# Kernel optimization log

Measured on AMD Instinct MI355X. Metric: run time of the kernel, lower is better.

The kernel has to match this reference:

```python
import jax, jax.numpy as jnp
import numpy as np

H = 128   # hidden_size
B = 8
TQ = 512  # num queries
TK = 512  # num keys


def setup_inputs() -> dict:
    key = jax.random.key(0)
    ks = jax.random.split(key, 8)
    s = 1.0 / np.sqrt(H)  # torch Linear default init bound
    return {
        "queries": jax.random.normal(ks[0], (B, TQ, H), dtype=jnp.float32),
        "keys": jax.random.normal(ks[1], (B, TK, H), dtype=jnp.float32),
        "Wa_w": jax.random.uniform(ks[2], (H, H), jnp.float32, -s, s),
        "Wa_b": jax.random.uniform(ks[3], (H,), jnp.float32, -s, s),
        "Ua_w": jax.random.uniform(ks[4], (H, H), jnp.float32, -s, s),
        "Ua_b": jax.random.uniform(ks[5], (H,), jnp.float32, -s, s),
        "Va_w": jax.random.uniform(ks[6], (H,), jnp.float32, -s, s),
        "Va_b": jax.random.uniform(ks[7], (), jnp.float32, -s, s),
    }


def reference(queries, keys, Wa_w, Wa_b, Ua_w, Ua_b, Va_w, Va_b):
    # Linear projections (torch Linear: y = x @ W.T + b)
    q = queries @ Wa_w.T + Wa_b                  # (B, Tq, H)
    k = keys @ Ua_w.T + Ua_b                     # (B, Tk, H)
    # Additive (Bahdanau) scores with broadcast intermediate (B, Tq, Tk, H)
    e = jnp.tanh(q[:, :, None, :] + k[:, None, :, :])
    scores = jnp.einsum('bqkh,h->bqk', e, Va_w) + Va_b  # (B, Tq, Tk)
    weights = jax.nn.softmax(scores, axis=-1)            # softmax over keys
    contexts = jnp.einsum('bqk,bkh->bqh', weights, keys) # (B, Tq, H)
    return contexts, weights
```

## Files before the change

kernel.cpp:

```cpp
#include <hip/hip_runtime.h>
#include <hip/hip_bf16.h>
#include <stdint.h>

#define HD 128
#define NB 8
#define TQN 512
#define TKN 512
#define QT 8
#define KTILE 64
#define KSTR 132
#define QSTR 132
#define KBSTR 136

typedef __attribute__((ext_vector_type(8))) short short8;
typedef __attribute__((ext_vector_type(4))) float f32x4;

static __device__ __forceinline__ float lo16(uint32_t w){
  union { uint32_t i; float f; } v; v.i = w << 16; return v.f;
}
static __device__ __forceinline__ float hi16(uint32_t w){
  union { uint32_t i; float f; } v; v.i = w & 0xffff0000u; return v.f;
}
static __device__ __forceinline__ float bf2f(unsigned short u){
  union { uint32_t i; float f; } v; v.i = ((uint32_t)u) << 16; return v.f;
}
static __device__ __forceinline__ uint32_t f2bf(float f){
  union { float f; uint32_t i; } v; v.f = f;
  uint32_t u = v.i;
  u += 0x7fffu + ((u >> 16) & 1u);
  return u >> 16;
}

static __device__ __forceinline__ float tanh_acc(float x){
  float e = __builtin_amdgcn_exp2f(x * 2.8853900817779268f);
  return fmaf(-2.0f, __builtin_amdgcn_rcpf(e + 1.0f), 1.0f);
}

template<int CTRL>
static __device__ __forceinline__ float dpp_add(float x){
  union { float f; int i; } u; u.f = x;
  int y = __builtin_amdgcn_update_dpp(0, u.i, CTRL, 0xf, 0xf, true);
  union { int i; float f; } w; w.i = y;
  return x + w.f;
}

static __device__ __forceinline__ float ld1(const void* p, size_t idx, bool f32){
  return f32 ? ((const float*)p)[idx] : bf2f(((const unsigned short*)p)[idx]);
}
static __device__ __forceinline__ short8 ld8bf(const void* p, size_t idx, bool f32){
  short8 r;
  if (f32){
    const float* s = (const float*)p + idx;
    #pragma unroll
    for (int i = 0; i < 8; i++) r[i] = (short)f2bf(s[i]);
  } else {
    r = *(const short8*)((const unsigned short*)p + idx);
  }
  return r;
}

static __device__ __forceinline__ void stage_keys(const void* keys, bool fK,
    unsigned short* keys_s, int b, int kt, int tid){
  if (fK){
    const float4* src = (const float4*)((const float*)keys + (size_t)(b*TKN + kt*KTILE)*HD);
    #pragma unroll
    for (int j = 0; j < 4; j++){
      const int f = tid + 512*j;
      float4 v = src[f];
      const int k = f >> 5;
      const int h = (f & 31) * 4;
      uint2 p;
      p.x = f2bf(v.x) | (f2bf(v.y) << 16);
      p.y = f2bf(v.z) | (f2bf(v.w) << 16);
      *(uint2*)(keys_s + k*KBSTR + h) = p;
    }
  } else {
    const uint4* src = (const uint4*)((const unsigned short*)keys + (size_t)(b*TKN + kt*KTILE)*HD);
    #pragma unroll
    for (int j = 0; j < 2; j++){
      const int f = tid + 512*j;
      uint4 v = src[f];
      const int k = f >> 4;
      const int h = (f & 15) * 8;
      *(uint4*)(keys_s + k*KBSTR + h) = v;
    }
  }
}

__global__ __launch_bounds__(512, 4) void fused_kernel(
    const void* __restrict__ queries, const void* __restrict__ keys,
    const void* __restrict__ Wa_w,   const void* __restrict__ Wa_b,
    const void* __restrict__ Ua_w,   const void* __restrict__ Ua_b,
    const void* __restrict__ Va_w,
    void* __restrict__ out)
{
  __shared__ float qp_s[QT*QSTR];
  __shared__ float va_s[HD];
  __shared__ __align__(16) unsigned short keys_s[KTILE*KBSTR];
  __shared__ __align__(16) float kp_s[KTILE*KSTR];
  __shared__ float sc_s[QT*TKN];
  __shared__ unsigned int flg_s[8];

  const int tid = threadIdx.x;

  if (tid < 8) flg_s[tid] = 0;
  __syncthreads();
  {
    const void* ptrs[7] = {queries, keys, Wa_w, Wa_b, Ua_w, Ua_b, Va_w};
    const int grp = tid >> 5;
    const int l   = tid & 31;
    if (grp < 7){
      const unsigned short* p = (const unsigned short*)ptrs[grp];
      unsigned short a = p[2*l];
      unsigned short c = p[64 + 2*l];
      if (((a >> 7) & 0xFF) > 0x90 || ((c >> 7) & 0xFF) > 0x90)
        atomicOr(&flg_s[grp], 1u);
    }
  }
  __syncthreads();
  const bool fQ  = flg_s[0] != 0;
  const bool fK  = flg_s[1] != 0;
  const bool fWw = flg_s[2] != 0;
  const bool fWb = flg_s[3] != 0;
  const bool fUw = flg_s[4] != 0;
  const bool fUb = flg_s[5] != 0;
  const bool fVw = flg_s[6] != 0;

  const int lane = tid & 63;
  const int wv   = tid >> 6;
  const int ln   = lane & 15;
  const int quad = lane >> 4;
  const int b     = blockIdx.x >> 6;
  const int qbase = (blockIdx.x & 63) * QT;

  if (tid < HD) va_s[tid] = ld1(Va_w, tid, fVw);

  {
    const int h0 = wv * 16;
    const size_t qrow = (size_t)(b*TQN + qbase + (ln & 7))*HD;
    f32x4 c = {0.f,0.f,0.f,0.f};
    #pragma unroll
    for (int ks = 0; ks < 4; ks++){
      short8 a = ld8bf(queries, qrow + ks*32 + quad*8, fQ);
      short8 w = ld8bf(Wa_w, (size_t)(h0 + ln)*HD + ks*32 + quad*8, fWw);
      c = __builtin_amdgcn_mfma_f32_16x16x32_bf16(a, w, c, 0,0,0);
    }
    const float wb = ld1(Wa_b, h0 + ln, fWb);
    #pragma unroll
    for (int r = 0; r < 4; r++){
      const int row = quad*4 + r;
      if (row < QT) qp_s[row*QSTR + h0 + ln] = tanh_acc(c[r] + wb);
    }
  }

  short8 ub[4];
  float ubias;
  {
    const int h0 = wv * 16;
    #pragma unroll
    for (int ks = 0; ks < 4; ks++)
      ub[ks] = ld8bf(Ua_w, (size_t)(h0 + ln)*HD + ks*32 + quad*8, fUw);
    ubias = ld1(Ua_b, h0 + ln, fUb);
  }

  stage_keys(keys, fK, keys_s, b, 0, tid);
  __syncthreads();

  const int s8 = lane >> 3;
  const int o8 = lane & 7;
  float tqr[16], var[16], vat[16];
  {
    const float* qsrc = qp_s + wv*QSTR + o8*16;
    const float* vsrc = va_s + o8*16;
    #pragma unroll
    for (int c = 0; c < 4; c++){
      float4 t = *(const float4*)(qsrc + c*4);
      float4 v = *(const float4*)(vsrc + c*4);
      tqr[c*4+0]=t.x; tqr[c*4+1]=t.y; tqr[c*4+2]=t.z; tqr[c*4+3]=t.w;
      var[c*4+0]=v.x; var[c*4+1]=v.y; var[c*4+2]=v.z; var[c*4+3]=v.w;
      vat[c*4+0]=v.x*t.x; vat[c*4+1]=v.y*t.y; vat[c*4+2]=v.z*t.z; vat[c*4+3]=v.w*t.w;
    }
  }

  for (int kt = 0; kt < 8; kt++){
    f32x4 kc[4];
    #pragma unroll
    for (int mt = 0; mt < 4; mt++) kc[mt] = (f32x4){0.f,0.f,0.f,0.f};
    #pragma unroll
    for (int ks = 0; ks < 4; ks++){
      short8 af[4];
      #pragma unroll
      for (int mt = 0; mt < 4; mt++)
        af[mt] = *(const short8*)(keys_s + (mt*16 + ln)*KBSTR + ks*32 + quad*8);
      #pragma unroll
      for (int mt = 0; mt < 4; mt++)
        kc[mt] = __builtin_amdgcn_mfma_f32_16x16x32_bf16(af[mt], ub[ks], kc[mt], 0,0,0);
    }
    __syncthreads();

    #pragma unroll
    for (int mt = 0; mt < 4; mt++)
      #pragma unroll
      for (int r = 0; r < 4; r++)
        kp_s[(mt*16 + quad*4 + r)*KSTR + wv*16 + ln] = tanh_acc(kc[mt][r] + ubias);
    if (kt < 7) stage_keys(keys, fK, keys_s, b, kt+1, tid);
    __syncthreads();

    float acc[8];
    #pragma unroll
    for (int i = 0; i < 8; i++) acc[i] = 0.f;
    #pragma unroll
    for (int i = 0; i < 8; i++){
      const float* tk = kp_s + (i*8 + s8)*KSTR + o8*16;
      #pragma unroll
      for (int c = 0; c < 4; c++){
        const float4 kv = *(const float4*)(tk + c*4);
        acc[i] = fmaf(fmaf(var[c*4+0], kv.x, vat[c*4+0]),
                      __builtin_amdgcn_rcpf(fmaf(tqr[c*4+0], kv.x, 1.f)), acc[i]);
        acc[i] = fmaf(fmaf(var[c*4+1], kv.y, vat[c*4+1]),
                      __builtin_amdgcn_rcpf(fmaf(tqr[c*4+1], kv.y, 1.f)), acc[i]);
        acc[i] = fmaf(fmaf(var[c*4+2], kv.z, vat[c*4+2]),
                      __builtin_amdgcn_rcpf(fmaf(tqr[c*4+2], kv.z, 1.f)), acc[i]);
        acc[i] = fmaf(fmaf(var[c*4+3], kv.w, vat[c*4+3]),
                      __builtin_amdgcn_rcpf(fmaf(tqr[c*4+3], kv.w, 1.f)), acc[i]);
      }
    }
    #pragma unroll
    for (int i = 0; i < 8; i++){
      float a = acc[i];
      a = dpp_add<0xB1>(a);
      a = dpp_add<0x4E>(a);
      a = dpp_add<0x141>(a);
      acc[i] = a;
    }
    float sc = acc[0];
    #pragma unroll
    for (int i = 1; i < 8; i++) sc = (o8 == i) ? acc[i] : sc;
    sc_s[wv*TKN + kt*KTILE + o8*8 + s8] = sc;
  }
  __syncthreads();

  {
    float vals[8];
    float m = -1e30f;
    #pragma unroll
    for (int j = 0; j < 8; j++){
      vals[j] = sc_s[wv*TKN + lane + 64*j];
      m = fmaxf(m, vals[j]);
    }
    #pragma unroll
    for (int o = 32; o > 0; o >>= 1) m = fmaxf(m, __shfl_xor(m, o));
    float sum = 0.f;
    #pragma unroll
    for (int j = 0; j < 8; j++){
      vals[j] = __builtin_amdgcn_exp2f((vals[j]-m)*1.4426950408889634f);
      sum += vals[j];
    }
    #pragma unroll
    for (int o = 32; o > 0; o >>= 1) sum += __shfl_xor(sum, o);
    const float inv = __builtin_amdgcn_rcpf(sum);
    const size_t wbase = (size_t)NB*TQN*HD + (size_t)(b*TQN + qbase + wv)*TKN;
    #pragma unroll
    for (int j = 0; j < 8; j++){
      const float w = vals[j]*inv;
      sc_s[wv*TKN + lane + 64*j] = w;
      if (fQ) ((float*)out)[wbase + lane + 64*j] = w;
      else    ((unsigned short*)out)[wbase + lane + 64*j] = (unsigned short)f2bf(w);
    }
  }
  __syncthreads();

  {
    const int p2 = wv & 3;
    const int g2 = wv >> 2;
    const int h0 = ln * 8;
    float a0[8], a1[8];
    #pragma unroll
    for (int t = 0; t < 8; t++){ a0[t] = 0.f; a1[t] = 0.f; }
    for (int kt = 0; kt < 8; kt++){
      if (fK){
        const float4* src = (const float4*)((const float*)keys + (size_t)(b*TKN + kt*KTILE)*HD);
        #pragma unroll
        for (int j = 0; j < 4; j++){
          const int f = tid + 512*j;
          const int k = f >> 5;
          const int h = (f & 31) * 4;
          *(float4*)(kp_s + k*KSTR + h) = src[f];
        }
      } else {
        const uint4* src = (const uint4*)((const unsigned short*)keys + (size_t)(b*TKN + kt*KTILE)*HD);
        #pragma unroll
        for (int j = 0; j < 2; j++){
          const int f = tid + 512*j;
          const int k = f >> 4;
          const int h = (f & 15) * 8;
          uint4 v = src[f];
          float4 d0, d1;
          d0.x = lo16(v.x); d0.y = hi16(v.x); d0.z = lo16(v.y); d0.w = hi16(v.y);
          d1.x = lo16(v.z); d1.y = hi16(v.z); d1.z = lo16(v.w); d1.w = hi16(v.w);
          *(float4*)(kp_s + k*KSTR + h)     = d0;
          *(float4*)(kp_s + k*KSTR + h + 4) = d1;
        }
      }
      __syncthreads();
      const float* w0r = sc_s + (2*p2)*TKN + kt*KTILE + g2*32;
      const float* w1r = w0r + TKN;
      #pragma unroll
      for (int i = 0; i < 8; i++){
        const int k = i*4 + quad;
        const float w0 = w0r[k];
        const float w1 = w1r[k];
        const float* kr = kp_s + (g2*32 + k)*KSTR + h0;
        const float4 k0 = *(const float4*)(kr);
        const float4 k1 = *(const float4*)(kr + 4);
        a0[0]=fmaf(w0,k0.x,a0[0]); a0[1]=fmaf(w0,k0.y,a0[1]);
        a0[2]=fmaf(w0,k0.z,a0[2]); a0[3]=fmaf(w0,k0.w,a0[3]);
        a0[4]=fmaf(w0,k1.x,a0[4]); a0[5]=fmaf(w0,k1.y,a0[5]);
        a0[6]=fmaf(w0,k1.z,a0[6]); a0[7]=fmaf(w0,k1.w,a0[7]);
        a1[0]=fmaf(w1,k0.x,a1[0]); a1[1]=fmaf(w1,k0.y,a1[1]);
        a1[2]=fmaf(w1,k0.z,a1[2]); a1[3]=fmaf(w1,k0.w,a1[3]);
        a1[4]=fmaf(w1,k1.x,a1[4]); a1[5]=fmaf(w1,k1.y,a1[5]);
        a1[6]=fmaf(w1,k1.z,a1[6]); a1[7]=fmaf(w1,k1.w,a1[7]);
      }
      __syncthreads();
    }
    #pragma unroll
    for (int t = 0; t < 8; t++){
      a0[t] += __shfl_xor(a0[t], 16); a0[t] += __shfl_xor(a0[t], 32);
      a1[t] += __shfl_xor(a1[t], 16); a1[t] += __shfl_xor(a1[t], 32);
    }
    float* part = qp_s;
    if (g2 == 1 && quad == 0){
      *(float4*)(part + (2*p2  )*HD + h0    ) = (float4){a0[0],a0[1],a0[2],a0[3]};
      *(float4*)(part + (2*p2  )*HD + h0 + 4) = (float4){a0[4],a0[5],a0[6],a0[7]};
      *(float4*)(part + (2*p2+1)*HD + h0    ) = (float4){a1[0],a1[1],a1[2],a1[3]};
      *(float4*)(part + (2*p2+1)*HD + h0 + 4) = (float4){a1[4],a1[5],a1[6],a1[7]};
    }
    __syncthreads();
    if (g2 == 0 && quad == 0){
      const float4 p00 = *(const float4*)(part + (2*p2  )*HD + h0    );
      const float4 p01 = *(const float4*)(part + (2*p2  )*HD + h0 + 4);
      const float4 p10 = *(const float4*)(part + (2*p2+1)*HD + h0    );
      const float4 p11 = *(const float4*)(part + (2*p2+1)*HD + h0 + 4);
      const size_t crow0 = (size_t)(b*TQN + qbase + 2*p2    )*HD + h0;
      const size_t crow1 = (size_t)(b*TQN + qbase + 2*p2 + 1)*HD + h0;
      if (fQ){
        float* oc = (float*)out;
        *(float4*)(oc + crow0)     = (float4){a0[0]+p00.x, a0[1]+p00.y, a0[2]+p00.z, a0[3]+p00.w};
        *(float4*)(oc + crow0 + 4) = (float4){a0[4]+p01.x, a0[5]+p01.y, a0[6]+p01.z, a0[7]+p01.w};
        *(float4*)(oc + crow1)     = (float4){a1[0]+p10.x, a1[1]+p10.y, a1[2]+p10.z, a1[3]+p10.w};
        *(float4*)(oc + crow1 + 4) = (float4){a1[4]+p11.x, a1[5]+p11.y, a1[6]+p11.z, a1[7]+p11.w};
      } else {
        uint4 o0, o1;
        o0.x = f2bf(a0[0]+p00.x) | (f2bf(a0[1]+p00.y) << 16);
        o0.y = f2bf(a0[2]+p00.z) | (f2bf(a0[3]+p00.w) << 16);
        o0.z = f2bf(a0[4]+p01.x) | (f2bf(a0[5]+p01.y) << 16);
        o0.w = f2bf(a0[6]+p01.z) | (f2bf(a0[7]+p01.w) << 16);
        o1.x = f2bf(a1[0]+p10.x) | (f2bf(a1[1]+p10.y) << 16);
        o1.y = f2bf(a1[2]+p10.z) | (f2bf(a1[3]+p10.w) << 16);
        o1.z = f2bf(a1[4]+p11.x) | (f2bf(a1[5]+p11.y) << 16);
        o1.w = f2bf(a1[6]+p11.z) | (f2bf(a1[7]+p11.w) << 16);
        *(uint4*)((unsigned short*)out + crow0) = o0;
        *(uint4*)((unsigned short*)out + crow1) = o1;
      }
    }
  }
}

extern "C" void kernel_launch(void* const* d_in, const int* in_sizes, int n_in,
                              void* d_out, int out_size, void* d_ws, size_t ws_size,
                              hipStream_t stream) {
  (void)in_sizes; (void)n_in; (void)out_size; (void)d_ws; (void)ws_size;
  fused_kernel<<<512, 512, 0, stream>>>(d_in[0], d_in[1], d_in[2], d_in[3],
                                        d_in[4], d_in[5], d_in[6], d_out);
}
```

Baseline: 158.4 us.

## Split projections into a separate kernel to avoid per-block key projection recompute

Moves the query and key linear projections plus tanh into a standalone proj_kernel that writes both to workspace once. The attention kernel then streams the precomputed tanh(k) tiles from global memory. Before, each of the 64 query blocks per batch recomputed the full key projection with MFMA. The score loop also drops the precomputed va*tq product in favour of computing va*(tq+k) inline. This costs an extra kernel launch and a global round trip of the fp32 projections, and lowers shared-memory use so the launch bound rises to 6 blocks. The old fused kernel stays as a fallback when the workspace is too small.

New measurement: 155.3 us. 1.02x faster.

```diff
diff --git a/kernel.cpp b/kernel.cpp
--- a/kernel.cpp
+++ b/kernel.cpp
@@ -30,12 +30,10 @@
   u += 0x7fffu + ((u >> 16) & 1u);
   return u >> 16;
 }
-
 static __device__ __forceinline__ float tanh_acc(float x){
   float e = __builtin_amdgcn_exp2f(x * 2.8853900817779268f);
   return fmaf(-2.0f, __builtin_amdgcn_rcpf(e + 1.0f), 1.0f);
 }
-
 template<int CTRL>
 static __device__ __forceinline__ float dpp_add(float x){
   union { float f; int i; } u; u.f = x;
@@ -43,7 +41,6 @@
   union { int i; float f; } w; w.i = y;
   return x + w.f;
 }
-
 static __device__ __forceinline__ float ld1(const void* p, size_t idx, bool f32){
   return f32 ? ((const float*)p)[idx] : bf2f(((const unsigned short*)p)[idx]);
 }
@@ -59,60 +56,81 @@
   return r;
 }
 
-static __device__ __forceinline__ void stage_keys(const void* keys, bool fK,
-    unsigned short* keys_s, int b, int kt, int tid){
-  if (fK){
-    const float4* src = (const float4*)((const float*)keys + (size_t)(b*TKN + kt*KTILE)*HD);
-    #pragma unroll
-    for (int j = 0; j < 4; j++){
-      const int f = tid + 512*j;
-      float4 v = src[f];
-      const int k = f >> 5;
-      const int h = (f & 31) * 4;
-      uint2 p;
-      p.x = f2bf(v.x) | (f2bf(v.y) << 16);
-      p.y = f2bf(v.z) | (f2bf(v.w) << 16);
-      *(uint2*)(keys_s + k*KBSTR + h) = p;
-    }
-  } else {
-    const uint4* src = (const uint4*)((const unsigned short*)keys + (size_t)(b*TKN + kt*KTILE)*HD);
-    #pragma unroll
-    for (int j = 0; j < 2; j++){
-      const int f = tid + 512*j;
-      uint4 v = src[f];
-      const int k = f >> 4;
-      const int h = (f & 15) * 8;
-      *(uint4*)(keys_s + k*KBSTR + h) = v;
-    }
-  }
-}
-
-__global__ __launch_bounds__(512, 4) void fused_kernel(
+__global__ __launch_bounds__(256) void proj_kernel(
     const void* __restrict__ queries, const void* __restrict__ keys,
     const void* __restrict__ Wa_w,   const void* __restrict__ Wa_b,
     const void* __restrict__ Ua_w,   const void* __restrict__ Ua_b,
+    float* __restrict__ tq_g, float* __restrict__ tk_g)
+{
+  __shared__ unsigned int flg_s[8];
+  const int tid = threadIdx.x;
+  if (tid < 8) flg_s[tid] = 0;
+  __syncthreads();
+  {
+    const void* ptrs[6] = {queries, keys, Wa_w, Wa_b, Ua_w, Ua_b};
+    const int grp = tid >> 5;
+    const int l   = tid & 31;
+    if (grp < 6){
+      const unsigned short* p = (const unsigned short*)ptrs[grp];
+      unsigned short a = p[2*l], c = p[64 + 2*l];
+      if (((a >> 7) & 0xFF) > 0x90 || ((c >> 7) & 0xFF) > 0x90)
+        atomicOr(&flg_s[grp], 1u);
+    }
+  }
+  __syncthreads();
+  const int lane = tid & 63, wv = tid >> 6, ln = lane & 15, quad = lane >> 4;
+  const int row0 = blockIdx.x * 16;
+
+  const void* x; const void* W; const void* bias; float* dst; int r;
+  bool fx, fw, fb;
+  if (row0 < NB*TQN){
+    x = queries; W = Wa_w; bias = Wa_b; dst = tq_g; r = row0;
+    fx = flg_s[0] != 0; fw = flg_s[2] != 0; fb = flg_s[3] != 0;
+  } else {
+    x = keys; W = Ua_w; bias = Ua_b; dst = tk_g; r = row0 - NB*TQN;
+    fx = flg_s[1] != 0; fw = flg_s[4] != 0; fb = flg_s[5] != 0;
+  }
+
+  short8 a[4];
+  #pragma unroll
+  for (int ks = 0; ks < 4; ks++)
+    a[ks] = ld8bf(x, (size_t)(r + ln)*HD + ks*32 + quad*8, fx);
+
+  #pragma unroll
+  for (int nt = 0; nt < 2; nt++){
+    const int h0 = (2*wv + nt)*16;
+    f32x4 c = {0.f,0.f,0.f,0.f};
+    #pragma unroll
+    for (int ks = 0; ks < 4; ks++)
+      c = __builtin_amdgcn_mfma_f32_16x16x32_bf16(
+            a[ks], ld8bf(W, (size_t)(h0 + ln)*HD + ks*32 + quad*8, fw), c, 0,0,0);
+    const float wb = ld1(bias, h0 + ln, fb);
+    #pragma unroll
+    for (int r4 = 0; r4 < 4; r4++)
+      dst[(size_t)(r + quad*4 + r4)*HD + h0 + ln] = tanh_acc(c[r4] + wb);
+  }
+}
+
+__global__ __launch_bounds__(512, 6) void attn_kernel(
+    const void* __restrict__ queries, const void* __restrict__ keys,
     const void* __restrict__ Va_w,
+    const float* __restrict__ tq_g, const float* __restrict__ tk_g,
     void* __restrict__ out)
 {
-  __shared__ float qp_s[QT*QSTR];
-  __shared__ float va_s[HD];
-  __shared__ __align__(16) unsigned short keys_s[KTILE*KBSTR];
-  __shared__ __align__(16) float kp_s[KTILE*KSTR];
+  __shared__ __align__(16) float tk_s[KTILE*KSTR];
   __shared__ float sc_s[QT*TKN];
-  __shared__ unsigned int flg_s[8];
+  __shared__ unsigned int flg_s[4];
 
   const int tid = threadIdx.x;
-
-  if (tid < 8) flg_s[tid] = 0;
-  __syncthreads();
-  {
-    const void* ptrs[7] = {queries, keys, Wa_w, Wa_b, Ua_w, Ua_b, Va_w};
+  if (tid < 4) flg_s[tid] = 0;
+  __syncthreads();
+  {
+    const void* ptrs[3] = {queries, keys, Va_w};
     const int grp = tid >> 5;
     const int l   = tid & 31;
-    if (grp < 7){
+    if (grp < 3){
       const unsigned short* p = (const unsigned short*)ptrs[grp];
-      unsigned short a = p[2*l];
-      unsigned short c = p[64 + 2*l];
+      unsigned short a = p[2*l], c = p[64 + 2*l];
       if (((a >> 7) & 0xFF) > 0x90 || ((c >> 7) & 0xFF) > 0x90)
         atomicOr(&flg_s[grp], 1u);
     }
@@ -120,108 +138,59 @@
   __syncthreads();
   const bool fQ  = flg_s[0] != 0;
   const bool fK  = flg_s[1] != 0;
-  const bool fWw = flg_s[2] != 0;
-  const bool fWb = flg_s[3] != 0;
-  const bool fUw = flg_s[4] != 0;
-  const bool fUb = flg_s[5] != 0;
-  const bool fVw = flg_s[6] != 0;
+  const bool fVw = flg_s[2] != 0;
 
   const int lane = tid & 63;
   const int wv   = tid >> 6;
   const int ln   = lane & 15;
   const int quad = lane >> 4;
+  const int s8   = lane >> 3;
+  const int o8   = lane & 7;
   const int b     = blockIdx.x >> 6;
   const int qbase = (blockIdx.x & 63) * QT;
 
-  if (tid < HD) va_s[tid] = ld1(Va_w, tid, fVw);
-
-  {
-    const int h0 = wv * 16;
-    const size_t qrow = (size_t)(b*TQN + qbase + (ln & 7))*HD;
-    f32x4 c = {0.f,0.f,0.f,0.f};
-    #pragma unroll
-    for (int ks = 0; ks < 4; ks++){
-      short8 a = ld8bf(queries, qrow + ks*32 + quad*8, fQ);
-      short8 w = ld8bf(Wa_w, (size_t)(h0 + ln)*HD + ks*32 + quad*8, fWw);
-      c = __builtin_amdgcn_mfma_f32_16x16x32_bf16(a, w, c, 0,0,0);
-    }
-    const float wb = ld1(Wa_b, h0 + ln, fWb);
-    #pragma unroll
-    for (int r = 0; r < 4; r++){
-      const int row = quad*4 + r;
-      if (row < QT) qp_s[row*QSTR + h0 + ln] = tanh_acc(c[r] + wb);
-    }
-  }
-
-  short8 ub[4];
-  float ubias;
-  {
-    const int h0 = wv * 16;
-    #pragma unroll
-    for (int ks = 0; ks < 4; ks++)
-      ub[ks] = ld8bf(Ua_w, (size_t)(h0 + ln)*HD + ks*32 + quad*8, fUw);
-    ubias = ld1(Ua_b, h0 + ln, fUb);
-  }
-
-  stage_keys(keys, fK, keys_s, b, 0, tid);
-  __syncthreads();
-
-  const int s8 = lane >> 3;
-  const int o8 = lane & 7;
-  float tqr[16], var[16], vat[16];
-  {
-    const float* qsrc = qp_s + wv*QSTR + o8*16;
-    const float* vsrc = va_s + o8*16;
+  float var[16], tqr[16];
+  {
+    #pragma unroll
+    for (int j = 0; j < 16; j++) var[j] = ld1(Va_w, o8*16 + j, fVw);
+    const float4* qsrc = (const float4*)(tq_g + (size_t)(b*TQN + qbase + wv)*HD + o8*16);
     #pragma unroll
     for (int c = 0; c < 4; c++){
-      float4 t = *(const float4*)(qsrc + c*4);
-      float4 v = *(const float4*)(vsrc + c*4);
+      float4 t = qsrc[c];
       tqr[c*4+0]=t.x; tqr[c*4+1]=t.y; tqr[c*4+2]=t.z; tqr[c*4+3]=t.w;
-      var[c*4+0]=v.x; var[c*4+1]=v.y; var[c*4+2]=v.z; var[c*4+3]=v.w;
-      vat[c*4+0]=v.x*t.x; vat[c*4+1]=v.y*t.y; vat[c*4+2]=v.z*t.z; vat[c*4+3]=v.w*t.w;
-    }
-  }
-
+    }
+  }
+
+  float sc8[8];
   for (int kt = 0; kt < 8; kt++){
-    f32x4 kc[4];
-    #pragma unroll
-    for (int mt = 0; mt < 4; mt++) kc[mt] = (f32x4){0.f,0.f,0.f,0.f};
-    #pragma unroll
-    for (int ks = 0; ks < 4; ks++){
-      short8 af[4];
-      #pragma unroll
-      for (int mt = 0; mt < 4; mt++)
-        af[mt] = *(const short8*)(keys_s + (mt*16 + ln)*KBSTR + ks*32 + quad*8);
-      #pragma unroll
-      for (int mt = 0; mt < 4; mt++)
-        kc[mt] = __builtin_amdgcn_mfma_f32_16x16x32_bf16(af[mt], ub[ks], kc[mt], 0,0,0);
+    {
+      const float4* src = (const float4*)(tk_g + (size_t)(b*TKN + kt*KTILE)*HD);
+      #pragma unroll
+      for (int j = 0; j < 4; j++){
+        const int f = tid + 512*j;
+        const int k = f >> 5;
+        const int h = (f & 31) * 4;
+        *(float4*)(tk_s + k*KSTR + h) = src[f];
+      }
     }
     __syncthreads();
 
-    #pragma unroll
-    for (int mt = 0; mt < 4; mt++)
-      #pragma unroll
-      for (int r = 0; r < 4; r++)
-        kp_s[(mt*16 + quad*4 + r)*KSTR + wv*16 + ln] = tanh_acc(kc[mt][r] + ubias);
-    if (kt < 7) stage_keys(keys, fK, keys_s, b, kt+1, tid);
-    __syncthreads();
-
     float acc[8];
     #pragma unroll
     for (int i = 0; i < 8; i++) acc[i] = 0.f;
     #pragma unroll
     for (int i = 0; i < 8; i++){
-      const float* tk = kp_s + (i*8 + s8)*KSTR + o8*16;
+      const float* tk = tk_s + (i*8 + s8)*KSTR + o8*16;
       #pragma unroll
       for (int c = 0; c < 4; c++){
         const float4 kv = *(const float4*)(tk + c*4);
-        acc[i] = fmaf(fmaf(var[c*4+0], kv.x, vat[c*4+0]),
+        acc[i] = fmaf(var[c*4+0]*(tqr[c*4+0]+kv.x),
                       __builtin_amdgcn_rcpf(fmaf(tqr[c*4+0], kv.x, 1.f)), acc[i]);
-        acc[i] = fmaf(fmaf(var[c*4+1], kv.y, vat[c*4+1]),
+        acc[i] = fmaf(var[c*4+1]*(tqr[c*4+1]+kv.y),
                       __builtin_amdgcn_rcpf(fmaf(tqr[c*4+1], kv.y, 1.f)), acc[i]);
-        acc[i] = fmaf(fmaf(var[c*4+2], kv.z, vat[c*4+2]),
+        acc[i] = fmaf(var[c*4+2]*(tqr[c*4+2]+kv.z),
                       __builtin_amdgcn_rcpf(fmaf(tqr[c*4+2], kv.z, 1.f)), acc[i]);
-        acc[i] = fmaf(fmaf(var[c*4+3], kv.w, vat[c*4+3]),
+        acc[i] = fmaf(var[c*4+3]*(tqr[c*4+3]+kv.w),
                       __builtin_amdgcn_rcpf(fmaf(tqr[c*4+3], kv.w, 1.f)), acc[i]);
       }
     }
@@ -236,25 +205,21 @@
     float sc = acc[0];
     #pragma unroll
     for (int i = 1; i < 8; i++) sc = (o8 == i) ? acc[i] : sc;
-    sc_s[wv*TKN + kt*KTILE + o8*8 + s8] = sc;
-  }
-  __syncthreads();
-
-  {
-    float vals[8];
-    float m = -1e30f;
-    #pragma unroll
-    for (int j = 0; j < 8; j++){
-      vals[j] = sc_s[wv*TKN + lane + 64*j];
-      m = fmaxf(m, vals[j]);
-    }
+    sc8[kt] = sc;
+    __syncthreads();
+  }
+
+  {
+    float m = sc8[0];
+    #pragma unroll
+    for (int j = 1; j < 8; j++) m = fmaxf(m, sc8[j]);
     #pragma unroll
     for (int o = 32; o > 0; o >>= 1) m = fmaxf(m, __shfl_xor(m, o));
     float sum = 0.f;
     #pragma unroll
     for (int j = 0; j < 8; j++){
-      vals[j] = __builtin_amdgcn_exp2f((vals[j]-m)*1.4426950408889634f);
-      sum += vals[j];
+      sc8[j] = __builtin_amdgcn_exp2f((sc8[j]-m)*1.4426950408889634f);
+      sum += sc8[j];
     }
     #pragma unroll
     for (int o = 32; o > 0; o >>= 1) sum += __shfl_xor(sum, o);
@@ -262,10 +227,11 @@
     const size_t wbase = (size_t)NB*TQN*HD + (size_t)(b*TQN + qbase + wv)*TKN;
     #pragma unroll
     for (int j = 0; j < 8; j++){
-      const float w = vals[j]*inv;
-      sc_s[wv*TKN + lane + 64*j] = w;
-      if (fQ) ((float*)out)[wbase + lane + 64*j] = w;
-      else    ((unsigned short*)out)[wbase + lane + 64*j] = (unsigned short)f2bf(w);
+      const float w = sc8[j]*inv;
+      const int kk = j*KTILE + o8*8 + s8;
+      sc_s[wv*TKN + kk] = w;
+      if (fQ) ((float*)out)[wbase + kk] = w;
+      else    ((unsigned short*)out)[wbase + kk] = (unsigned short)f2bf(w);
     }
   }
   __syncthreads();
@@ -285,7 +251,7 @@
           const int f = tid + 512*j;
           const int k = f >> 5;
           const int h = (f & 31) * 4;
-          *(float4*)(kp_s + k*KSTR + h) = src[f];
+          *(float4*)(tk_s + k*KSTR + h) = src[f];
         }
       } else {
         const uint4* src = (const uint4*)((const unsigned short*)keys + (size_t)(b*TKN + kt*KTILE)*HD);
@@ -298,8 +264,8 @@
           float4 d0, d1;
           d0.x = lo16(v.x); d0.y = hi16(v.x); d0.z = lo16(v.y); d0.w = hi16(v.y);
           d1.x = lo16(v.z); d1.y = hi16(v.z); d1.z = lo16(v.w); d1.w = hi16(v.w);
-          *(float4*)(kp_s + k*KSTR + h)     = d0;
-          *(float4*)(kp_s + k*KSTR + h + 4) = d1;
+          *(float4*)(tk_s + k*KSTR + h)     = d0;
+          *(float4*)(tk_s + k*KSTR + h + 4) = d1;
         }
       }
       __syncthreads();
@@ -310,7 +276,7 @@
         const int k = i*4 + quad;
         const float w0 = w0r[k];
         const float w1 = w1r[k];
-        const float* kr = kp_s + (g2*32 + k)*KSTR + h0;
+        const float* kr = tk_s + (g2*32 + k)*KSTR + h0;
         const float4 k0 = *(const float4*)(kr);
         const float4 k1 = *(const float4*)(kr + 4);
         a0[0]=fmaf(w0,k0.x,a0[0]); a0[1]=fmaf(w0,k0.y,a0[1]);
@@ -329,7 +295,7 @@
       a0[t] += __shfl_xor(a0[t], 16); a0[t] += __shfl_xor(a0[t], 32);
       a1[t] += __shfl_xor(a1[t], 16); a1[t] += __shfl_xor(a1[t], 32);
     }
-    float* part = qp_s;
+    float* part = sc_s;
     if (g2 == 1 && quad == 0){
       *(float4*)(part + (2*p2  )*HD + h0    ) = (float4){a0[0],a0[1],a0[2],a0[3]};
       *(float4*)(part + (2*p2  )*HD + h0 + 4) = (float4){a0[4],a0[5],a0[6],a0[7]};
@@ -367,10 +333,334 @@
   }
 }
 
+__global__ __launch_bounds__(512, 4) void fused_kernel(
+    const void* __restrict__ queries, const void* __restrict__ keys,
+    const void* __restrict__ Wa_w,   const void* __restrict__ Wa_b,
+    const void* __restrict__ Ua_w,   const void* __restrict__ Ua_b,
+    const void* __restrict__ Va_w,
+    void* __restrict__ out)
+{
+  __shared__ float qp_s[QT*QSTR];
+  __shared__ float va_s[HD];
+  __shared__ __align__(16) unsigned short keys_s[KTILE*KBSTR];
+  __shared__ __align__(16) float kp_s[KTILE*KSTR];
+  __shared__ float sc_s[QT*TKN];
+  __shared__ unsigned int flg_s[8];
+
+  const int tid = threadIdx.x;
+  if (tid < 8) flg_s[tid] = 0;
+  __syncthreads();
+  {
+    const void* ptrs[7] = {queries, keys, Wa_w, Wa_b, Ua_w, Ua_b, Va_w};
+    const int grp = tid >> 5;
+    const int l   = tid & 31;
+    if (grp < 7){
+      const unsigned short* p = (const unsigned short*)ptrs[grp];
+      unsigned short a = p[2*l], c = p[64 + 2*l];
+      if (((a >> 7) & 0xFF) > 0x90 || ((c >> 7) & 0xFF) > 0x90)
+        atomicOr(&flg_s[grp], 1u);
+    }
+  }
+  __syncthreads();
+  const bool fQ  = flg_s[0] != 0;
+  const bool fK  = flg_s[1] != 0;
+  const bool fWw = flg_s[2] != 0;
+  const bool fWb = flg_s[3] != 0;
+  const bool fUw = flg_s[4] != 0;
+  const bool fUb = flg_s[5] != 0;
+  const bool fVw = flg_s[6] != 0;
+
+  const int lane = tid & 63;
+  const int wv   = tid >> 6;
+  const int ln   = lane & 15;
+  const int quad = lane >> 4;
+  const int b     = blockIdx.x >> 6;
+  const int qbase = (blockIdx.x & 63) * QT;
+
+  if (tid < HD) va_s[tid] = ld1(Va_w, tid, fVw);
+  {
+    const int h0 = wv * 16;
+    const size_t qrow = (size_t)(b*TQN + qbase + (ln & 7))*HD;
+    f32x4 c = {0.f,0.f,0.f,0.f};
+    #pragma unroll
+    for (int ks = 0; ks < 4; ks++){
+      short8 a = ld8bf(queries, qrow + ks*32 + quad*8, fQ);
+      short8 w = ld8bf(Wa_w, (size_t)(h0 + ln)*HD + ks*32 + quad*8, fWw);
+      c = __builtin_amdgcn_mfma_f32_16x16x32_bf16(a, w, c, 0,0,0);
+    }
+    const float wb = ld1(Wa_b, h0 + ln, fWb);
+    #pragma unroll
+    for (int r = 0; r < 4; r++){
+      const int row = quad*4 + r;
+      if (row < QT) qp_s[row*QSTR + h0 + ln] = tanh_acc(c[r] + wb);
+    }
+  }
+  short8 ub[4];
+  float ubias;
+  {
+    const int h0 = wv * 16;
+    #pragma unroll
+    for (int ks = 0; ks < 4; ks++)
+      ub[ks] = ld8bf(Ua_w, (size_t)(h0 + ln)*HD + ks*32 + quad*8, fUw);
+    ubias = ld1(Ua_b, h0 + ln, fUb);
+  }
+  {
+    if (fK){
+      const float4* src = (const float4*)((const float*)keys + (size_t)(b*TKN)*HD);
+      #pragma unroll
+      for (int j = 0; j < 4; j++){
+        const int f = tid + 512*j;
+        float4 v = src[f];
+        const int k = f >> 5, h = (f & 31)*4;
+        uint2 p;
+        p.x = f2bf(v.x) | (f2bf(v.y) << 16);
+        p.y = f2bf(v.z) | (f2bf(v.w) << 16);
+        *(uint2*)(keys_s + k*KBSTR + h) = p;
+      }
+    } else {
+      const uint4* src = (const uint4*)((const unsigned short*)keys + (size_t)(b*TKN)*HD);
+      #pragma unroll
+      for (int j = 0; j < 2; j++){
+        const int f = tid + 512*j;
+        uint4 v = src[f];
+        const int k = f >> 4, h = (f & 15)*8;
+        *(uint4*)(keys_s + k*KBSTR + h) = v;
+      }
+    }
+  }
+  __syncthreads();
+
+  const int s8 = lane >> 3;
+  const int o8 = lane & 7;
+  float tqr[16], var[16], vat[16];
+  {
+    const float* qsrc = qp_s + wv*QSTR + o8*16;
+    const float* vsrc = va_s + o8*16;
+    #pragma unroll
+    for (int c = 0; c < 4; c++){
+      float4 t = *(const float4*)(qsrc + c*4);
+      float4 v = *(const float4*)(vsrc + c*4);
+      tqr[c*4+0]=t.x; tqr[c*4+1]=t.y; tqr[c*4+2]=t.z; tqr[c*4+3]=t.w;
+      var[c*4+0]=v.x; var[c*4+1]=v.y; var[c*4+2]=v.z; var[c*4+3]=v.w;
+      vat[c*4+0]=v.x*t.x; vat[c*4+1]=v.y*t.y; vat[c*4+2]=v.z*t.z; vat[c*4+3]=v.w*t.w;
+    }
+  }
+  for (int kt = 0; kt < 8; kt++){
+    f32x4 kc[4];
+    #pragma unroll
+    for (int mt = 0; mt < 4; mt++) kc[mt] = (f32x4){0.f,0.f,0.f,0.f};
+    #pragma unroll
+    for (int ks = 0; ks < 4; ks++){
+      short8 af[4];
+      #pragma unroll
+      for (int mt = 0; mt < 4; mt++)
+        af[mt] = *(const short8*)(keys_s + (mt*16 + ln)*KBSTR + ks*32 + quad*8);
+      #pragma unroll
+      for (int mt = 0; mt < 4; mt++)
+        kc[mt] = __builtin_amdgcn_mfma_f32_16x16x32_bf16(af[mt], ub[ks], kc[mt], 0,0,0);
+    }
+    __syncthreads();
+    #pragma unroll
+    for (int mt = 0; mt < 4; mt++)
+      #pragma unroll
+      for (int r = 0; r < 4; r++)
+        kp_s[(mt*16 + quad*4 + r)*KSTR + wv*16 + ln] = tanh_acc(kc[mt][r] + ubias);
+    if (kt < 7){
+      if (fK){
+        const float4* src = (const float4*)((const float*)keys + (size_t)(b*TKN + (kt+1)*KTILE)*HD);
+        #pragma unroll
+        for (int j = 0; j < 4; j++){
+          const int f = tid + 512*j;
+          float4 v = src[f];
+          const int k = f >> 5, h = (f & 31)*4;
+          uint2 p;
+          p.x = f2bf(v.x) | (f2bf(v.y) << 16);
+          p.y = f2bf(v.z) | (f2bf(v.w) << 16);
+          *(uint2*)(keys_s + k*KBSTR + h) = p;
+        }
+      } else {
+        const uint4* src = (const uint4*)((const unsigned short*)keys + (size_t)(b*TKN + (kt+1)*KTILE)*HD);
+        #pragma unroll
+        for (int j = 0; j < 2; j++){
+          const int f = tid + 512*j;
+          uint4 v = src[f];
+          const int k = f >> 4, h = (f & 15)*8;
+          *(uint4*)(keys_s + k*KBSTR + h) = v;
+        }
+      }
+    }
+    __syncthreads();
+    float acc[8];
+    #pragma unroll
+    for (int i = 0; i < 8; i++) acc[i] = 0.f;
+    #pragma unroll
+    for (int i = 0; i < 8; i++){
+      const float* tk = kp_s + (i*8 + s8)*KSTR + o8*16;
+      #pragma unroll
+      for (int c = 0; c < 4; c++){
+        const float4 kv = *(const float4*)(tk + c*4);
+        acc[i] = fmaf(fmaf(var[c*4+0], kv.x, vat[c*4+0]),
+                      __builtin_amdgcn_rcpf(fmaf(tqr[c*4+0], kv.x, 1.f)), acc[i]);
+        acc[i] = fmaf(fmaf(var[c*4+1], kv.y, vat[c*4+1]),
+                      __builtin_amdgcn_rcpf(fmaf(tqr[c*4+1], kv.y, 1.f)), acc[i]);
+        acc[i] = fmaf(fmaf(var[c*4+2], kv.z, vat[c*4+2]),
+                      __builtin_amdgcn_rcpf(fmaf(tqr[c*4+2], kv.z, 1.f)), acc[i]);
+        acc[i] = fmaf(fmaf(var[c*4+3], kv.w, vat[c*4+3]),
+                      __builtin_amdgcn_rcpf(fmaf(tqr[c*4+3], kv.w, 1.f)), acc[i]);
+      }
+    }
+    #pragma unroll
+    for (int i = 0; i < 8; i++){
+      float a = acc[i];
+      a = dpp_add<0xB1>(a);
+      a = dpp_add<0x4E>(a);
+      a = dpp_add<0x141>(a);
+      acc[i] = a;
+    }
+    float sc = acc[0];
+    #pragma unroll
+    for (int i = 1; i < 8; i++) sc = (o8 == i) ? acc[i] : sc;
+    sc_s[wv*TKN + kt*KTILE + o8*8 + s8] = sc;
+  }
+  __syncthreads();
+  {
+    float vals[8];
+    float m = -1e30f;
+    #pragma unroll
+    for (int j = 0; j < 8; j++){
+      vals[j] = sc_s[wv*TKN + lane + 64*j];
+      m = fmaxf(m, vals[j]);
+    }
+    #pragma unroll
+    for (int o = 32; o > 0; o >>= 1) m = fmaxf(m, __shfl_xor(m, o));
+    float sum = 0.f;
+    #pragma unroll
+    for (int j = 0; j < 8; j++){
+      vals[j] = __builtin_amdgcn_exp2f((vals[j]-m)*1.4426950408889634f);
+      sum += vals[j];
+    }
+    #pragma unroll
+    for (int o = 32; o > 0; o >>= 1) sum += __shfl_xor(sum, o);
+    const float inv = __builtin_amdgcn_rcpf(sum);
+    const size_t wbase = (size_t)NB*TQN*HD + (size_t)(b*TQN + qbase + wv)*TKN;
+    #pragma unroll
+    for (int j = 0; j < 8; j++){
+      const float w = vals[j]*inv;
+      sc_s[wv*TKN + lane + 64*j] = w;
+      if (fQ) ((float*)out)[wbase + lane + 64*j] = w;
+      else    ((unsigned short*)out)[wbase + lane + 64*j] = (unsigned short)f2bf(w);
+    }
+  }
+  __syncthreads();
+  {
+    const int p2 = wv & 3;
+    const int g2 = wv >> 2;
+    const int h0 = ln * 8;
+    float a0[8], a1[8];
+    #pragma unroll
+    for (int t = 0; t < 8; t++){ a0[t] = 0.f; a1[t] = 0.f; }
+    for (int kt = 0; kt < 8; kt++){
+      if (fK){
+        const float4* src = (const float4*)((const float*)keys + (size_t)(b*TKN + kt*KTILE)*HD);
+        #pragma unroll
+        for (int j = 0; j < 4; j++){
+          const int f = tid + 512*j;
+          const int k = f >> 5, h = (f & 31)*4;
+          *(float4*)(kp_s + k*KSTR + h) = src[f];
+        }
+      } else {
+        const uint4* src = (const uint4*)((const unsigned short*)keys + (size_t)(b*TKN + kt*KTILE)*HD);
+        #pragma unroll
+        for (int j = 0; j < 2; j++){
+          const int f = tid + 512*j;
+          const int k = f >> 4, h = (f & 15)*8;
+          uint4 v = src[f];
+          float4 d0, d1;
+          d0.x = lo16(v.x); d0.y = hi16(v.x); d0.z = lo16(v.y); d0.w = hi16(v.y);
+          d1.x = lo16(v.z); d1.y = hi16(v.z); d1.z = lo16(v.w); d1.w = hi16(v.w);
+          *(float4*)(kp_s + k*KSTR + h)     = d0;
+          *(float4*)(kp_s + k*KSTR + h + 4) = d1;
+        }
+      }
+      __syncthreads();
+      const float* w0r = sc_s + (2*p2)*TKN + kt*KTILE + g2*32;
+      const float* w1r = w0r + TKN;
+      #pragma unroll
+      for (int i = 0; i < 8; i++){
+        const int k = i*4 + quad;
+        const float w0 = w0r[k];
+        const float w1 = w1r[k];
+        const float* kr = kp_s + (g2*32 + k)*KSTR + h0;
+        const float4 k0 = *(const float4*)(kr);
+        const float4 k1 = *(const float4*)(kr + 4);
+        a0[0]=fmaf(w0,k0.x,a0[0]); a0[1]=fmaf(w0,k0.y,a0[1]);
+        a0[2]=fmaf(w0,k0.z,a0[2]); a0[3]=fmaf(w0,k0.w,a0[3]);
+        a0[4]=fmaf(w0,k1.x,a0[4]); a0[5]=fmaf(w0,k1.y,a0[5]);
+        a0[6]=fmaf(w0,k1.z,a0[6]); a0[7]=fmaf(w0,k1.w,a0[7]);
+        a1[0]=fmaf(w1,k0.x,a1[0]); a1[1]=fmaf(w1,k0.y,a1[1]);
+        a1[2]=fmaf(w1,k0.z,a1[2]); a1[3]=fmaf(w1,k0.w,a1[3]);
+        a1[4]=fmaf(w1,k1.x,a1[4]); a1[5]=fmaf(w1,k1.y,a1[5]);
+        a1[6]=fmaf(w1,k1.z,a1[6]); a1[7]=fmaf(w1,k1.w,a1[7]);
+      }
+      __syncthreads();
+    }
+    #pragma unroll
+    for (int t = 0; t < 8; t++){
+      a0[t] += __shfl_xor(a0[t], 16); a0[t] += __shfl_xor(a0[t], 32);
+      a1[t] += __shfl_xor(a1[t], 16); a1[t] += __shfl_xor(a1[t], 32);
+    }
+    float* part = qp_s;
+    if (g2 == 1 && quad == 0){
+      *(float4*)(part + (2*p2  )*HD + h0    ) = (float4){a0[0],a0[1],a0[2],a0[3]};
+      *(float4*)(part + (2*p2  )*HD + h0 + 4) = (float4){a0[4],a0[5],a0[6],a0[7]};
+      *(float4*)(part + (2*p2+1)*HD + h0    ) = (float4){a1[0],a1[1],a1[2],a1[3]};
+      *(float4*)(part + (2*p2+1)*HD + h0 + 4) = (float4){a1[4],a1[5],a1[6],a1[7]};
+    }
+    __syncthreads();
+    if (g2 == 0 && quad == 0){
+      const float4 p00 = *(const float4*)(part + (2*p2  )*HD + h0    );
+      const float4 p01 = *(const float4*)(part + (2*p2  )*HD + h0 + 4);
+      const float4 p10 = *(const float4*)(part + (2*p2+1)*HD + h0    );
+      const float4 p11 = *(const float4*)(part + (2*p2+1)*HD + h0 + 4);
+      const size_t crow0 = (size_t)(b*TQN + qbase + 2*p2    )*HD + h0;
+      const size_t crow1 = (size_t)(b*TQN + qbase + 2*p2 + 1)*HD + h0;
+      if (fQ){
+        float* oc = (float*)out;
+        *(float4*)(oc + crow0)     = (float4){a0[0]+p00.x, a0[1]+p00.y, a0[2]+p00.z, a0[3]+p00.w};
+        *(float4*)(oc + crow0 + 4) = (float4){a0[4]+p01.x, a0[5]+p01.y, a0[6]+p01.z, a0[7]+p01.w};
+        *(float4*)(oc + crow1)     = (float4){a1[0]+p10.x, a1[1]+p10.y, a1[2]+p10.z, a1[3]+p10.w};
+        *(float4*)(oc + crow1 + 4) = (float4){a1[4]+p11.x, a1[5]+p11.y, a1[6]+p11.z, a1[7]+p11.w};
+      } else {
+        uint4 o0, o1;
+        o0.x = f2bf(a0[0]+p00.x) | (f2bf(a0[1]+p00.y) << 16);
+        o0.y = f2bf(a0[2]+p00.z) | (f2bf(a0[3]+p00.w) << 16);
+        o0.z = f2bf(a0[4]+p01.x) | (f2bf(a0[5]+p01.y) << 16);
+        o0.w = f2bf(a0[6]+p01.z) | (f2bf(a0[7]+p01.w) << 16);
+        o1.x = f2bf(a1[0]+p10.x) | (f2bf(a1[1]+p10.y) << 16);
+        o1.y = f2bf(a1[2]+p10.z) | (f2bf(a1[3]+p10.w) << 16);
+        o1.z = f2bf(a1[4]+p11.x) | (f2bf(a1[5]+p11.y) << 16);
+        o1.w = f2bf(a1[6]+p11.z) | (f2bf(a1[7]+p11.w) << 16);
+        *(uint4*)((unsigned short*)out + crow0) = o0;
+        *(uint4*)((unsigned short*)out + crow1) = o1;
+      }
+    }
+  }
+}
+
 extern "C" void kernel_launch(void* const* d_in, const int* in_sizes, int n_in,
                               void* d_out, int out_size, void* d_ws, size_t ws_size,
                               hipStream_t stream) {
-  (void)in_sizes; (void)n_in; (void)out_size; (void)d_ws; (void)ws_size;
-  fused_kernel<<<512, 512, 0, stream>>>(d_in[0], d_in[1], d_in[2], d_in[3],
-                                        d_in[4], d_in[5], d_in[6], d_out);
-}
+  (void)in_sizes; (void)n_in; (void)out_size;
+  const size_t need = (size_t)2 * NB * TQN * HD * sizeof(float);
+  if (ws_size >= need){
+    float* tq_g = (float*)d_ws;
+    float* tk_g = tq_g + (size_t)NB*TQN*HD;
+    proj_kernel<<<512, 256, 0, stream>>>(d_in[0], d_in[1], d_in[2], d_in[3],
+                                         d_in[4], d_in[5], tq_g, tk_g);
+    attn_kernel<<<512, 512, 0, stream>>>(d_in[0], d_in[1], d_in[6],
+                                         tq_g, tk_g, d_out);
+  } else {
+    fused_kernel<<<512, 512, 0, stream>>>(d_in[0], d_in[1], d_in[2], d_in[3],
+                                          d_in[4], d_in[5], d_in[6], d_out);
+  }
+}
```
